# Optimization experiments

Measured on AMD Instinct MI355X. Metric: run time of the kernel, lower is better.

The kernel has to match this reference:

```python
import jax, jax.numpy as jnp
import numpy as np

DIM = 768; NL = 13; NH = 12; VOCAB = 50257; SEQ = 512; B = 4
HID = 4 * DIM; HD = DIM // NH; LUT_SIZE = 256


def setup_inputs() -> dict:
    key = jax.random.key(0)
    ks = jax.random.split(key, 10)
    def n(k, shape, s=0.02):
        return jax.random.normal(k, shape, jnp.float32) * s
    return {
        'lut': jnp.linspace(-0.1, 0.1, LUT_SIZE, dtype=jnp.float32),  # 256-entry primal codebook
        'tok_emb': n(ks[0], (VOCAB, DIM)),
        'pos_emb': n(ks[1], (SEQ, DIM)),
        'ln1_g': jnp.ones((NL, DIM), jnp.float32), 'ln1_b': jnp.zeros((NL, DIM), jnp.float32),
        'in_w': n(ks[2], (NL, 3 * DIM, DIM)), 'in_b': jnp.zeros((NL, 3 * DIM), jnp.float32),
        'out_w': n(ks[3], (NL, DIM, DIM)), 'out_b': jnp.zeros((NL, DIM), jnp.float32),
        'ln2_g': jnp.ones((NL, DIM), jnp.float32), 'ln2_b': jnp.zeros((NL, DIM), jnp.float32),
        'mlp1_scale': jnp.ones((NL, HID, 1), jnp.float32),
        'mlp2_scale': jnp.ones((NL, DIM, 1), jnp.float32),
        'lnf_g': jnp.ones((DIM,), jnp.float32), 'lnf_b': jnp.zeros((DIM,), jnp.float32),
        'head_scale': jnp.ones((VOCAB, 1), jnp.float32),
        'mlp1_idx': jax.random.randint(ks[4], (NL, HID, DIM), 0, LUT_SIZE, jnp.int32),
        'mlp2_idx': jax.random.randint(ks[5], (NL, DIM, HID), 0, LUT_SIZE, jnp.int32),
        'head_idx': jax.random.randint(ks[6], (VOCAB, DIM), 0, LUT_SIZE, jnp.int32),
        'idx': jax.random.randint(ks[7], (B, SEQ), 0, VOCAB, jnp.int32),
    }


def layernorm(x, g, b, eps=1e-5):
    m = jnp.mean(x, -1, keepdims=True)
    v = jnp.var(x, -1, keepdims=True)
    return (x - m) * jax.lax.rsqrt(v + eps) * g + b


def ghost_linear(x, gidx, scale, lut):
    # dequantize: gather codebook values, row-scale, then matmul (no bias)
    w = lut[gidx] * scale  # [out, in]
    return x @ w.T


def mha(x, wi, bi, wo, bo, mask):
    Bn, T, D = x.shape
    qkv = x @ wi.T + bi
    q, k, v = jnp.split(qkv, 3, axis=-1)
    q = q.reshape(Bn, T, NH, HD); k = k.reshape(Bn, T, NH, HD); v = v.reshape(Bn, T, NH, HD)
    s = jnp.einsum('bqhd,bkhd->bhqk', q, k) / jnp.sqrt(jnp.float32(HD)) + mask
    a = jax.nn.softmax(s, axis=-1)
    o = jnp.einsum('bhqk,bkhd->bqhd', a, v).reshape(Bn, T, D)
    return o @ wo.T + bo


def reference(lut, tok_emb, pos_emb, ln1_g, ln1_b, in_w, in_b, out_w, out_b,
              ln2_g, ln2_b, mlp1_scale, mlp2_scale, lnf_g, lnf_b, head_scale,
              mlp1_idx, mlp2_idx, head_idx, idx):
    Bn, T = idx.shape
    x = tok_emb[idx] + pos_emb[:T]
    causal = jnp.triu(jnp.ones((T, T), bool), 1)
    mask = jnp.where(causal, -jnp.inf, 0.0).astype(jnp.float32)
    for l in range(NL):
        h = layernorm(x, ln1_g[l], ln1_b[l])
        x = x + mha(h, in_w[l], in_b[l], out_w[l], out_b[l], mask)
        h = layernorm(x, ln2_g[l], ln2_b[l])
        h = ghost_linear(h, mlp1_idx[l], mlp1_scale[l], lut)
        h = jax.nn.gelu(h, approximate=True)  # GELU tanh approximation
        x = x + ghost_linear(h, mlp2_idx[l], mlp2_scale[l], lut)
    x = layernorm(x, lnf_g, lnf_b)
    return ghost_linear(x, head_idx, head_scale, lut)
```

## Files before the change

### kernel.cpp

```cpp
#include <hip/hip_runtime.h>
#include <stdint.h>

#define DIM 768
#define NL 13
#define NH 12
#define VOCAB 50257
#define SEQ 512
#define BATCH 4
#define HID 3072
#define HD 64
#define NTOK (BATCH*SEQ)
#define BHB (BATCH*NH)

typedef unsigned short u16;
typedef __attribute__((ext_vector_type(8))) __bf16 bf16x8;
typedef __attribute__((ext_vector_type(4))) float f32x4;

__device__ __forceinline__ u16 f2bf(float f) {
    union { float f; uint32_t u; } v; v.f = f;
    uint32_t u = v.u;
    return (u16)((u + 0x7FFFu + ((u >> 16) & 1u)) >> 16);
}

__device__ __forceinline__ void gl2lds16(const void* g, void* l) {
    __builtin_amdgcn_global_load_lds((const __attribute__((address_space(1))) void*)g,
                                     (__attribute__((address_space(3))) void*)l,
                                     16, 0, 0);
}

__device__ __forceinline__ float gelu_tanh(float x) {
    float x3 = x * x * x;
    float t = tanhf(0.7978845608028654f * (x + 0.044715f * x3));
    return 0.5f * x * (1.0f + t);
}

template<int EPI>
__device__ __forceinline__ void epi_store(float v, int r, int c, int N, int z, long sC,
                                          const float* bias, const float* resid,
                                          void* out0, void* out1, void* out2)
{
    if constexpr (EPI == 0) {
        if (c < N) ((float*)out0)[(long)z * sC + (long)r * N + c] = v;
    } else if constexpr (EPI == 1) {
        v += bias[c];
        const int part = c / DIM;
        const int cc = c - part * DIM;
        const int hh = cc >> 6, d = cc & 63;
        const int b = r >> 9, t = r & 511;
        const int bh = b * NH + hh;
        if (part == 0)      ((u16*)out0)[((long)bh * SEQ + t) * HD + d] = f2bf(v);
        else if (part == 1) ((u16*)out1)[((long)bh * SEQ + t) * HD + d] = f2bf(v);
        else                ((u16*)out2)[((long)bh * HD + d) * SEQ + t] = f2bf(v);
    } else if constexpr (EPI == 3) {
        if (bias) v += bias[c];
        v += resid[(long)r * N + c];
        ((float*)out0)[(long)r * N + c] = v;
    } else {
        ((u16*)out0)[(long)r * N + c] = f2bf(gelu_tanh(v));
    }
}

template<int WN, int EPI>
__global__ __launch_bounds__(256)
void gemm_bt(const u16* __restrict__ A, const u16* __restrict__ B,
             const float* __restrict__ bias, const float* __restrict__ resid,
             void* __restrict__ out0, void* __restrict__ out1, void* __restrict__ out2,
             int M, int N, int K, long sA, long sB, long sC)
{
    constexpr int TN = WN * 32;
    __shared__ __align__(16) u16 As[2 * 128 * 32];
    __shared__ __align__(16) u16 Bs[2 * TN * 32];

    const int tid  = threadIdx.x;
    const int wave = tid >> 6;
    const int lane = tid & 63;
    const int quad = lane >> 4;
    const int l16  = lane & 15;
    const int wm   = wave >> 1;
    const int wn   = wave & 1;

    int bx = blockIdx.x, by = blockIdx.y;
    {
        const int gx = gridDim.x;
        const int nwg = gx * gridDim.y;
        const int orig = by * gx + bx;
        const int xcd = orig & 7;
        const int q = nwg >> 3, r = nwg & 7;
        const int wg = (xcd < r ? xcd * (q + 1) : r * (q + 1) + (xcd - r) * q) + (orig >> 3);
        bx = wg % gx; by = wg / gx;
    }

    const int m0 = bx * 128;
    const int n0 = by * TN;
    const int z  = blockIdx.z;

    const u16* Ab = A + (long)z * sA;
    const u16* Bb = B + (long)z * sB;

    const int srow = tid >> 2;
    const int scol = ((tid & 3) ^ ((srow >> 1) & 3)) * 8;

    u16* const asw0 = As + wave * 512;
    u16* const asw1 = As + 2048 + wave * 512;
    u16* const bsw0 = Bs + wave * 512;
    u16* const bsw1 = Bs + 2048 + wave * 512;

    const long aoff0 = (long)(m0 + srow) * K + scol;
    const long aoff1 = (long)(m0 + 64 + srow) * K + scol;
    int br0 = n0 + srow;      if (br0 > N - 1) br0 = N - 1;
    int br1 = n0 + 64 + srow; if (br1 > N - 1) br1 = N - 1;
    const long boff0 = (long)br0 * K + scol;
    const long boff1 = (long)br1 * K + scol;

    auto stage = [&](int b, int k0) {
        const int ao = b * 4096;
        const int bo = b * (TN * 32);
        gl2lds16(Ab + aoff0 + k0, asw0 + ao);
        gl2lds16(Ab + aoff1 + k0, asw1 + ao);
        gl2lds16(Bb + boff0 + k0, bsw0 + bo);
        if constexpr (WN == 4) gl2lds16(Bb + boff1 + k0, bsw1 + bo);
    };

    f32x4 acc[4][WN];
    #pragma unroll
    for (int i = 0; i < 4; i++)
        #pragma unroll
        for (int j = 0; j < WN; j++)
            acc[i][j] = (f32x4){0.f, 0.f, 0.f, 0.f};

    const int sq8 = (quad ^ ((l16 >> 1) & 3)) * 8;
    const int arow = (wm * 64 + l16) * 32 + sq8;
    const int brow = (wn * (WN * 16) + l16) * 32 + sq8;

    stage(0, 0);
    __syncthreads();

    int cur = 0;
    for (int k0 = 0; k0 < K; k0 += 32) {
        if (k0 + 32 < K) stage(cur ^ 1, k0 + 32);

        const u16* Ar = As + cur * 4096;
        const u16* Br = Bs + cur * (TN * 32);
        bf16x8 af[4], bfr[WN];
        #pragma unroll
        for (int i = 0; i < 4; i++)
            af[i] = *(const bf16x8*)&Ar[arow + i * 512];
        #pragma unroll
        for (int j = 0; j < WN; j++)
            bfr[j] = *(const bf16x8*)&Br[brow + j * 512];
        #pragma unroll
        for (int i = 0; i < 4; i++)
            #pragma unroll
            for (int j = 0; j < WN; j++)
                acc[i][j] = __builtin_amdgcn_mfma_f32_16x16x32_bf16(af[i], bfr[j], acc[i][j], 0, 0, 0);

        __syncthreads();
        cur ^= 1;
    }

    const int rbase = m0 + wm * 64;
    const int cbase = n0 + wn * (WN * 16);
    #pragma unroll
    for (int i = 0; i < 4; i++)
        #pragma unroll
        for (int j = 0; j < WN; j++)
            #pragma unroll
            for (int rg = 0; rg < 4; rg++)
                epi_store<EPI>(acc[i][j][rg], rbase + i * 16 + quad * 4 + rg,
                               cbase + j * 16 + l16, N, z, sC, bias, resid, out0, out1, out2);
}

template<int WN, int EPI>
__global__ __launch_bounds__(256)
void gemm_bt_s(const u16* __restrict__ A, const u16* __restrict__ B,
               const float* __restrict__ bias, const float* __restrict__ resid,
               void* __restrict__ out0, void* __restrict__ out1, void* __restrict__ out2,
               int M, int N, int K)
{
    constexpr int TN = WN * 32;
    __shared__ __align__(16) u16 As[2 * 64 * 32];
    __shared__ __align__(16) u16 Bs[2 * TN * 32];

    const int tid  = threadIdx.x;
    const int wave = tid >> 6;
    const int lane = tid & 63;
    const int quad = lane >> 4;
    const int l16  = lane & 15;
    const int wm   = wave >> 1;
    const int wn   = wave & 1;

    int bx = blockIdx.x, by = blockIdx.y;
    {
        const int gx = gridDim.x;
        const int nwg = gx * gridDim.y;
        const int orig = by * gx + bx;
        const int xcd = orig & 7;
        const int q = nwg >> 3, r = nwg & 7;
        const int wg = (xcd < r ? xcd * (q + 1) : r * (q + 1) + (xcd - r) * q) + (orig >> 3);
        bx = wg % gx; by = wg / gx;
    }

    const int m0 = bx * 64;
    const int n0 = by * TN;

    const int srow = tid >> 2;
    const int scol = ((tid & 3) ^ ((srow >> 1) & 3)) * 8;

    u16* const asw  = As + wave * 512;
    u16* const bsw0 = Bs + wave * 512;
    u16* const bsw1 = Bs + 2048 + wave * 512;

    const long aoff = (long)(m0 + srow) * K + scol;
    int br0 = n0 + srow;      if (br0 > N - 1) br0 = N - 1;
    int br1 = n0 + 64 + srow; if (br1 > N - 1) br1 = N - 1;
    const long boff0 = (long)br0 * K + scol;
    const long boff1 = (long)br1 * K + scol;

    auto stage = [&](int b, int k0) {
        gl2lds16(A + aoff + k0, asw + b * 2048);
        gl2lds16(B + boff0 + k0, bsw0 + b * (TN * 32));
        if constexpr (WN == 4) gl2lds16(B + boff1 + k0, bsw1 + b * (TN * 32));
    };

    f32x4 acc[2][WN];
    #pragma unroll
    for (int i = 0; i < 2; i++)
        #pragma unroll
        for (int j = 0; j < WN; j++)
            acc[i][j] = (f32x4){0.f, 0.f, 0.f, 0.f};

    const int sq8 = (quad ^ ((l16 >> 1) & 3)) * 8;
    const int arow = (wm * 32 + l16) * 32 + sq8;
    const int brow = (wn * (WN * 16) + l16) * 32 + sq8;

    stage(0, 0);
    __syncthreads();

    int cur = 0;
    for (int k0 = 0; k0 < K; k0 += 32) {
        if (k0 + 32 < K) stage(cur ^ 1, k0 + 32);

        const u16* Ar = As + cur * 2048;
        const u16* Br = Bs + cur * (TN * 32);
        bf16x8 af[2], bfr[WN];
        #pragma unroll
        for (int i = 0; i < 2; i++)
            af[i] = *(const bf16x8*)&Ar[arow + i * 512];
        #pragma unroll
        for (int j = 0; j < WN; j++)
            bfr[j] = *(const bf16x8*)&Br[brow + j * 512];
        #pragma unroll
        for (int i = 0; i < 2; i++)
            #pragma unroll
            for (int j = 0; j < WN; j++)
                acc[i][j] = __builtin_amdgcn_mfma_f32_16x16x32_bf16(af[i], bfr[j], acc[i][j], 0, 0, 0);

        __syncthreads();
        cur ^= 1;
    }

    const int rbase = m0 + wm * 32;
    const int cbase = n0 + wn * (WN * 16);
    #pragma unroll
    for (int i = 0; i < 2; i++)
        #pragma unroll
        for (int j = 0; j < WN; j++)
            #pragma unroll
            for (int rg = 0; rg < 4; rg++)
                epi_store<EPI>(acc[i][j][rg], rbase + i * 16 + quad * 4 + rg,
                               cbase + j * 16 + l16, N, 0, 0, bias, resid, out0, out1, out2);
}

__global__ __launch_bounds__(256)
void attn_kernel(const u16* __restrict__ qb, const u16* __restrict__ kb,
                 const u16* __restrict__ vtb, u16* __restrict__ ob)
{
    __shared__ __align__(16) u16 Ks[512 * 64];
    __shared__ __align__(16) u16 Vs[64 * 512];
    __shared__ __align__(16) u16 Ps[4][32 * 64];

    const int tid  = threadIdx.x;
    const int wave = tid >> 6;
    const int lane = tid & 63;
    const int quad = lane >> 4;
    const int l16  = lane & 15;

    const int bh   = blockIdx.x;
    const int qblk = blockIdx.y;
    const int qr0  = qblk * 128 + wave * 32;

    #pragma unroll 4
    for (int cI = 0; cI < 16; ++cI) {
        const int rbase = cI * 32 + wave * 8;
        const int r  = rbase + (lane >> 3);
        const int ch = lane & 7;
        gl2lds16(kb + ((long)bh * SEQ + r) * HD + ((ch ^ (r & 7)) * 8), Ks + rbase * 64);
    }
    #pragma unroll 4
    for (int cI = 0; cI < 16; ++cI) {
        const int d = cI * 4 + wave;
        gl2lds16(vtb + ((long)bh * HD + d) * SEQ + ((lane ^ (d & 7)) * 8), Vs + d * 512);
    }

    bf16x8 af[2][2];
    const long qoff = ((long)bh * SEQ + qr0) * HD;
    #pragma unroll
    for (int i = 0; i < 2; i++)
        #pragma unroll
        for (int kc = 0; kc < 2; kc++)
            af[i][kc] = *(const bf16x8*)&qb[qoff + (long)(i * 16 + l16) * HD + kc * 32 + quad * 8];

    __syncthreads();

    f32x4 o[2][4];
    float mrun[2][4], lrun[2][4];
    #pragma unroll
    for (int i = 0; i < 2; i++)
        #pragma unroll
        for (int rg = 0; rg < 4; rg++) { mrun[i][rg] = -1e30f; lrun[i][rg] = 0.f; }
    #pragma unroll
    for (int i = 0; i < 2; i++)
        #pragma unroll
        for (int nd = 0; nd < 4; nd++)
            o[i][nd] = (f32x4){0.f, 0.f, 0.f, 0.f};

    u16* const Pw = &Ps[wave][0];
    const int rsw = l16 & 7;
    const int kvend = qr0 + 32;

    for (int kv0 = 0; kv0 < kvend; kv0 += 64) {
        f32x4 s[2][4];
        #pragma unroll
        for (int i = 0; i < 2; i++)
            #pragma unroll
            for (int n = 0; n < 4; n++)
                s[i][n] = (f32x4){0.f, 0.f, 0.f, 0.f};
        bf16x8 bf[4][2];
        #pragma unroll
        for (int n = 0; n < 4; n++)
            #pragma unroll
            for (int kc = 0; kc < 2; kc++)
                bf[n][kc] = *(const bf16x8*)&Ks[(kv0 + n * 16 + l16) * 64 + (((kc * 4 + quad) ^ rsw) * 8)];
        #pragma unroll
        for (int i = 0; i < 2; i++)
            #pragma unroll
            for (int n = 0; n < 4; n++)
                #pragma unroll
                for (int kc = 0; kc < 2; kc++)
                    s[i][n] = __builtin_amdgcn_mfma_f32_16x16x32_bf16(af[i][kc], bf[n][kc], s[i][n], 0, 0, 0);

        #pragma unroll
        for (int i = 0; i < 2; i++) {
            #pragma unroll
            for (int rg = 0; rg < 4; rg++) {
                const int q = qr0 + i * 16 + quad * 4 + rg;
                float v[4];
                #pragma unroll
                for (int n = 0; n < 4; n++) {
                    const int c = kv0 + n * 16 + l16;
                    v[n] = (c <= q) ? s[i][n][rg] * 0.125f : -1e30f;
                }
                float pm = fmaxf(fmaxf(v[0], v[1]), fmaxf(v[2], v[3]));
                #pragma unroll
                for (int off = 1; off < 16; off <<= 1) pm = fmaxf(pm, __shfl_xor(pm, off));
                const float mo = mrun[i][rg];
                const float mn = fmaxf(mo, pm);
                const float corr = __expf(mo - mn);
                float ps = 0.f;
                #pragma unroll
                for (int n = 0; n < 4; n++) { const float e = __expf(v[n] - mn); v[n] = e; ps += e; }
                #pragma unroll
                for (int off = 1; off < 16; off <<= 1) ps += __shfl_xor(ps, off);
                lrun[i][rg] = lrun[i][rg] * corr + ps;
                mrun[i][rg] = mn;
                #pragma unroll
                for (int nd = 0; nd < 4; nd++) o[i][nd][rg] *= corr;
                const int qlz = i * 16 + quad * 4 + rg;
                const int sw = qlz & 7;
                #pragma unroll
                for (int n = 0; n < 4; n++)
                    Pw[qlz * 64 + (((n * 2 + (l16 >> 3)) ^ sw) * 8) + (l16 & 7)] = f2bf(v[n]);
            }
        }
        asm volatile("s_waitcnt lgkmcnt(0)" ::: "memory");

        bf16x8 pa[2][2], vb[4][2];
        #pragma unroll
        for (int i = 0; i < 2; i++)
            #pragma unroll
            for (int kc = 0; kc < 2; kc++)
                pa[i][kc] = *(const bf16x8*)&Pw[(i * 16 + l16) * 64 + (((kc * 4 + quad) ^ rsw) * 8)];
        #pragma unroll
        for (int nd = 0; nd < 4; nd++)
            #pragma unroll
            for (int kc = 0; kc < 2; kc++)
                vb[nd][kc] = *(const bf16x8*)&Vs[(nd * 16 + l16) * 512 + ((((kv0 >> 3) + kc * 4 + quad) ^ rsw) * 8)];
        #pragma unroll
        for (int i = 0; i < 2; i++)
            #pragma unroll
            for (int nd = 0; nd < 4; nd++)
                #pragma unroll
                for (int kc = 0; kc < 2; kc++)
                    o[i][nd] = __builtin_amdgcn_mfma_f32_16x16x32_bf16(pa[i][kc], vb[nd][kc], o[i][nd], 0, 0, 0);
    }

    const int b  = bh / NH, hh = bh - b * NH;
    #pragma unroll
    for (int i = 0; i < 2; i++) {
        #pragma unroll
        for (int rg = 0; rg < 4; rg++) {
            const float inv = 1.f / lrun[i][rg];
            const int t = qr0 + i * 16 + quad * 4 + rg;
            u16* orow = ob + ((long)(b * SEQ + t)) * DIM + hh * HD;
            #pragma unroll
            for (int nd = 0; nd < 4; nd++)
                orow[nd * 16 + l16] = f2bf(o[i][nd][rg] * inv);
        }
    }
}

__global__ __launch_bounds__(256)
void embed_kernel(const int* __restrict__ tokidx, const float* __restrict__ tok,
                  const float* __restrict__ pos, float* __restrict__ x)
{
    const int i = blockIdx.x * 256 + threadIdx.x;
    const int row = i / 192;
    const int c4 = i - row * 192;
    const int t = row & (SEQ - 1);
    const int tk = tokidx[row];
    const float4 a = *(const float4*)&tok[(long)tk * DIM + c4 * 4];
    const float4 p = *(const float4*)&pos[(long)t * DIM + c4 * 4];
    *(float4*)&x[(long)row * DIM + c4 * 4] = make_float4(a.x + p.x, a.y + p.y, a.z + p.z, a.w + p.w);
}

__global__ __launch_bounds__(256)
void ln_kernel(const float* __restrict__ x, const float* __restrict__ g,
               const float* __restrict__ b, u16* __restrict__ out)
{
    const int row = blockIdx.x * 4 + (threadIdx.x >> 6);
    const int lane = threadIdx.x & 63;
    const float* xr = x + (long)row * DIM;
    float v[12];
    float s = 0.f, s2 = 0.f;
    #pragma unroll
    for (int i = 0; i < 3; i++) {
        const float4 f = *(const float4*)&xr[i * 256 + lane * 4];
        v[i*4+0] = f.x; v[i*4+1] = f.y; v[i*4+2] = f.z; v[i*4+3] = f.w;
        s  += f.x + f.y + f.z + f.w;
        s2 += f.x*f.x + f.y*f.y + f.z*f.z + f.w*f.w;
    }
    for (int o = 32; o; o >>= 1) { s += __shfl_xor(s, o); s2 += __shfl_xor(s2, o); }
    const float m  = s * (1.f / DIM);
    const float var = s2 * (1.f / DIM) - m * m;
    const float rs = rsqrtf(var + 1e-5f);
    u16* orow = out + (long)row * DIM;
    #pragma unroll
    for (int i = 0; i < 3; i++) {
        const int c = i * 256 + lane * 4;
        ushort4 o4 = make_ushort4(
            f2bf((v[i*4+0] - m) * rs * g[c+0] + b[c+0]),
            f2bf((v[i*4+1] - m) * rs * g[c+1] + b[c+1]),
            f2bf((v[i*4+2] - m) * rs * g[c+2] + b[c+2]),
            f2bf((v[i*4+3] - m) * rs * g[c+3] + b[c+3]));
        *(ushort4*)&orow[c] = o4;
    }
}

__global__ __launch_bounds__(256)
void tobf16_kernel(const float* __restrict__ in, u16* __restrict__ out)
{
    const long i = ((long)blockIdx.x * 256 + threadIdx.x) * 4;
    const float4 f = *(const float4*)&in[i];
    *(ushort4*)&out[i] = make_ushort4(f2bf(f.x), f2bf(f.y), f2bf(f.z), f2bf(f.w));
}

__global__ __launch_bounds__(256)
void dequant_kernel(const int* __restrict__ gidx, const float* __restrict__ scale,
                    const float* __restrict__ lut, u16* __restrict__ w,
                    long total, int Kd)
{
    __shared__ float slut[256];
    slut[threadIdx.x] = lut[threadIdx.x];
    __syncthreads();
    const long i4 = ((long)blockIdx.x * 256 + threadIdx.x) * 4;
    if (i4 >= total) return;
    const int4 g = *(const int4*)&gidx[i4];
    const float sc = scale[(int)(i4 / Kd)];
    *(ushort4*)&w[i4] = make_ushort4(f2bf(slut[g.x] * sc), f2bf(slut[g.y] * sc),
                                     f2bf(slut[g.z] * sc), f2bf(slut[g.w] * sc));
}

extern "C" void kernel_launch(void* const* d_in, const int* in_sizes, int n_in,
                              void* d_out, int out_size, void* d_ws, size_t ws_size,
                              hipStream_t stream)
{
    const float* lut        = (const float*)d_in[0];
    const float* tok_emb    = (const float*)d_in[1];
    const float* pos_emb    = (const float*)d_in[2];
    const float* ln1_g      = (const float*)d_in[3];
    const float* ln1_b      = (const float*)d_in[4];
    const float* in_w       = (const float*)d_in[5];
    const float* in_b       = (const float*)d_in[6];
    const float* out_w      = (const float*)d_in[7];
    const float* out_b      = (const float*)d_in[8];
    const float* ln2_g      = (const float*)d_in[9];
    const float* ln2_b      = (const float*)d_in[10];
    const float* mlp1_scale = (const float*)d_in[11];
    const float* mlp2_scale = (const float*)d_in[12];
    const float* lnf_g      = (const float*)d_in[13];
    const float* lnf_b      = (const float*)d_in[14];
    const float* head_scale = (const float*)d_in[15];
    const int*   mlp1_idx   = (const int*)d_in[16];
    const int*   mlp2_idx   = (const int*)d_in[17];
    const int*   head_idx   = (const int*)d_in[18];
    const int*   tokids     = (const int*)d_in[19];

    char* p = (char*)d_ws;
    auto alloc = [&](size_t bytes) { char* r = p; p += (bytes + 255) & ~(size_t)255; return r; };
    float* x    = (float*)alloc((size_t)NTOK * DIM * 4);
    u16*  h     = (u16*) alloc((size_t)NTOK * DIM * 2);
    u16*  h2    = (u16*) alloc((size_t)NTOK * HID * 2);
    u16*  qb    = (u16*) alloc((size_t)BHB * SEQ * HD * 2);
    u16*  kb    = (u16*) alloc((size_t)BHB * SEQ * HD * 2);
    u16*  vtb   = (u16*) alloc((size_t)BHB * SEQ * HD * 2);
    u16*  ob    = (u16*) alloc((size_t)NTOK * DIM * 2);
    u16*  inw16 = (u16*) alloc((size_t)NL * 3 * DIM * DIM * 2);
    u16*  outw16= (u16*) alloc((size_t)NL * DIM * DIM * 2);
    u16*  w1    = (u16*) alloc((size_t)HID * DIM * 2);
    u16*  w2    = (u16*) alloc((size_t)DIM * HID * 2);
    u16*  hw    = (u16*) alloc((size_t)VOCAB * DIM * 2);

    embed_kernel<<<NTOK * 192 / 256, 256, 0, stream>>>(tokids, tok_emb, pos_emb, x);
    tobf16_kernel<<<NL * 3 * DIM * DIM / 1024, 256, 0, stream>>>(in_w, inw16);
    tobf16_kernel<<<NL * DIM * DIM / 1024, 256, 0, stream>>>(out_w, outw16);
    {
        const long total = (long)VOCAB * DIM;
        const int blocks = (int)((total / 4 + 255) / 256);
        dequant_kernel<<<blocks, 256, 0, stream>>>(head_idx, head_scale, lut, hw, total, DIM);
    }

    for (int l = 0; l < NL; l++) {
        ln_kernel<<<NTOK / 4, 256, 0, stream>>>(x, ln1_g + l * DIM, ln1_b + l * DIM, h);
        gemm_bt_s<4, 1><<<dim3(NTOK / 64, 3 * DIM / 128), 256, 0, stream>>>(
            h, inw16 + (long)l * 3 * DIM * DIM, in_b + l * 3 * DIM, nullptr,
            qb, kb, vtb, NTOK, 3 * DIM, DIM);
        attn_kernel<<<dim3(BHB, 4), 256, 0, stream>>>(qb, kb, vtb, ob);
        gemm_bt_s<2, 3><<<dim3(NTOK / 64, DIM / 64), 256, 0, stream>>>(
            ob, outw16 + (long)l * DIM * DIM, out_b + l * DIM, x,
            x, nullptr, nullptr, NTOK, DIM, DIM);
        ln_kernel<<<NTOK / 4, 256, 0, stream>>>(x, ln2_g + l * DIM, ln2_b + l * DIM, h);
        dequant_kernel<<<HID * DIM / 1024, 256, 0, stream>>>(
            mlp1_idx + (long)l * HID * DIM, mlp1_scale + l * HID, lut, w1, (long)HID * DIM, DIM);
        gemm_bt_s<4, 4><<<dim3(NTOK / 64, HID / 128), 256, 0, stream>>>(
            h, w1, nullptr, nullptr, h2, nullptr, nullptr, NTOK, HID, DIM);
        dequant_kernel<<<DIM * HID / 1024, 256, 0, stream>>>(
            mlp2_idx + (long)l * DIM * HID, mlp2_scale + l * DIM, lut, w2, (long)DIM * HID, HID);
        gemm_bt_s<2, 3><<<dim3(NTOK / 64, DIM / 64), 256, 0, stream>>>(
            h2, w2, nullptr, x, x, nullptr, nullptr, NTOK, DIM, HID);
    }

    ln_kernel<<<NTOK / 4, 256, 0, stream>>>(x, lnf_g, lnf_b, h);
    gemm_bt<4, 0><<<dim3(NTOK / 128, (VOCAB + 127) / 128, 1), 256, 0, stream>>>(
        h, hw, nullptr, nullptr, d_out, nullptr, nullptr, NTOK, VOCAB, DIM, 0, 0, 0);
}
```

Measured before the change: 2.935 ms.

## Fuse LUT dequantization into MLP GEMMs and widen K-tile to 64

Removes the separate per-layer dequant kernels for the MLP weights. The GEMM now loads int32 codebook indices straight from global memory, looks them up in an LDS-resident LUT, applies the row scale, converts to bf16 and writes the result into shared memory, with the loads software-pipelined against the MFMA loop. The K tile grows from 32 to 64 with a new 8-way XOR swizzle, which halves the number of barriers per K. In exchange, every M-tile block re-reads and re-dequantizes the int32 indices, which are 4 bytes per weight, so global traffic for the weights rises unless L2 absorbs it.

Result: slower. 3.222 ms (+9.8%).

```diff
diff --git a/kernel.cpp b/kernel.cpp
--- a/kernel.cpp
+++ b/kernel.cpp
@@ -32,6 +32,16 @@
     float x3 = x * x * x;
     float t = tanhf(0.7978845608028654f * (x + 0.044715f * x3));
     return 0.5f * x * (1.0f + t);
+}
+
+__device__ __forceinline__ void xcd_remap(int& bx, int& by) {
+    const int gx = gridDim.x;
+    const int nwg = gx * gridDim.y;
+    const int orig = by * gx + bx;
+    const int xcd = orig & 7;
+    const int q = nwg >> 3, r = nwg & 7;
+    const int wg = (xcd < r ? xcd * (q + 1) : r * (q + 1) + (xcd - r) * q) + (orig >> 3);
+    bx = wg % gx; by = wg / gx;
 }
 
 template<int EPI>
@@ -80,15 +90,7 @@
     const int wn   = wave & 1;
 
     int bx = blockIdx.x, by = blockIdx.y;
-    {
-        const int gx = gridDim.x;
-        const int nwg = gx * gridDim.y;
-        const int orig = by * gx + bx;
-        const int xcd = orig & 7;
-        const int q = nwg >> 3, r = nwg & 7;
-        const int wg = (xcd < r ? xcd * (q + 1) : r * (q + 1) + (xcd - r) * q) + (orig >> 3);
-        bx = wg % gx; by = wg / gx;
-    }
+    xcd_remap(bx, by);
 
     const int m0 = bx * 128;
     const int n0 = by * TN;
@@ -170,16 +172,19 @@
                                cbase + j * 16 + l16, N, z, sC, bias, resid, out0, out1, out2);
 }
 
-template<int WN, int EPI>
+template<int WN, int EPI, bool GHOST>
 __global__ __launch_bounds__(256)
-void gemm_bt_s(const u16* __restrict__ A, const u16* __restrict__ B,
-               const float* __restrict__ bias, const float* __restrict__ resid,
-               void* __restrict__ out0, void* __restrict__ out1, void* __restrict__ out2,
-               int M, int N, int K)
+void gemm64(const u16* __restrict__ A, const void* __restrict__ Bsrc,
+            const float* __restrict__ scale, const float* __restrict__ lutg,
+            const float* __restrict__ bias, const float* __restrict__ resid,
+            void* __restrict__ out0, void* __restrict__ out1, void* __restrict__ out2,
+            int M, int N, int K)
 {
     constexpr int TN = WN * 32;
-    __shared__ __align__(16) u16 As[2 * 64 * 32];
-    __shared__ __align__(16) u16 Bs[2 * TN * 32];
+    constexpr int NC = TN / 32;
+    __shared__ __align__(16) u16 As[2 * 64 * 64];
+    __shared__ __align__(16) u16 Bs[2 * TN * 64];
+    __shared__ float slut[256];
 
     const int tid  = threadIdx.x;
     const int wave = tid >> 6;
@@ -190,36 +195,59 @@
     const int wn   = wave & 1;
 
     int bx = blockIdx.x, by = blockIdx.y;
-    {
-        const int gx = gridDim.x;
-        const int nwg = gx * gridDim.y;
-        const int orig = by * gx + bx;
-        const int xcd = orig & 7;
-        const int q = nwg >> 3, r = nwg & 7;
-        const int wg = (xcd < r ? xcd * (q + 1) : r * (q + 1) + (xcd - r) * q) + (orig >> 3);
-        bx = wg % gx; by = wg / gx;
-    }
-
+    xcd_remap(bx, by);
     const int m0 = bx * 64;
     const int n0 = by * TN;
 
-    const int srow = tid >> 2;
-    const int scol = ((tid & 3) ^ ((srow >> 1) & 3)) * 8;
-
-    u16* const asw  = As + wave * 512;
-    u16* const bsw0 = Bs + wave * 512;
-    u16* const bsw1 = Bs + 2048 + wave * 512;
-
-    const long aoff = (long)(m0 + srow) * K + scol;
-    int br0 = n0 + srow;      if (br0 > N - 1) br0 = N - 1;
-    int br1 = n0 + 64 + srow; if (br1 > N - 1) br1 = N - 1;
-    const long boff0 = (long)br0 * K + scol;
-    const long boff1 = (long)br1 * K + scol;
-
-    auto stage = [&](int b, int k0) {
-        gl2lds16(A + aoff + k0, asw + b * 2048);
-        gl2lds16(B + boff0 + k0, bsw0 + b * (TN * 32));
-        if constexpr (WN == 4) gl2lds16(B + boff1 + k0, bsw1 + b * (TN * 32));
+    if constexpr (GHOST) slut[tid] = lutg[tid];
+
+    const int srow = tid >> 3;
+    const int sch  = ((tid & 7) ^ (srow & 7)) * 8;
+    u16* const asw = As + wave * 512;
+
+    const long aoff = (long)(m0 + srow) * K + sch;
+    auto stageA = [&](int b, int k0) {
+        #pragma unroll
+        for (int c = 0; c < 2; c++)
+            gl2lds16(A + aoff + (long)c * 32 * K + k0, asw + b * 4096 + c * 2048);
+    };
+
+    const u16* const Bw = (const u16*)Bsrc;
+    u16* const bsw = Bs + wave * 512;
+    const long boff = (long)(n0 + srow) * K + sch;
+    auto stageB = [&](int b, int k0) {
+        #pragma unroll
+        for (int c = 0; c < NC; c++)
+            gl2lds16(Bw + boff + (long)c * 32 * K + k0, bsw + b * TN * 64 + c * 2048);
+    };
+
+    const int* const gidx = (const int*)Bsrc;
+    int4 gq[NC][2];
+    float bsc[NC];
+    if constexpr (GHOST) {
+        #pragma unroll
+        for (int c = 0; c < NC; c++) bsc[c] = scale[n0 + c * 32 + srow];
+    }
+    auto ghostLoad = [&](int k0) {
+        #pragma unroll
+        for (int c = 0; c < NC; c++) {
+            const long o = (long)(n0 + c * 32 + srow) * K + k0 + (tid & 7) * 8;
+            gq[c][0] = *(const int4*)&gidx[o];
+            gq[c][1] = *(const int4*)&gidx[o + 4];
+        }
+    };
+    auto ghostWrite = [&](int b) {
+        #pragma unroll
+        for (int c = 0; c < NC; c++) {
+            const float s = bsc[c];
+            uint32_t p0 = (uint32_t)f2bf(slut[gq[c][0].x] * s) | ((uint32_t)f2bf(slut[gq[c][0].y] * s) << 16);
+            uint32_t p1 = (uint32_t)f2bf(slut[gq[c][0].z] * s) | ((uint32_t)f2bf(slut[gq[c][0].w] * s) << 16);
+            uint32_t p2 = (uint32_t)f2bf(slut[gq[c][1].x] * s) | ((uint32_t)f2bf(slut[gq[c][1].y] * s) << 16);
+            uint32_t p3 = (uint32_t)f2bf(slut[gq[c][1].z] * s) | ((uint32_t)f2bf(slut[gq[c][1].w] * s) << 16);
+            u16* dst = Bs + b * TN * 64 + (c * 32 + srow) * 64 + sch;
+            uint4 w; w.x = p0; w.y = p1; w.z = p2; w.w = p3;
+            *(uint4*)dst = w;
+        }
     };
 
     f32x4 acc[2][WN];
@@ -229,32 +257,50 @@
         for (int j = 0; j < WN; j++)
             acc[i][j] = (f32x4){0.f, 0.f, 0.f, 0.f};
 
-    const int sq8 = (quad ^ ((l16 >> 1) & 3)) * 8;
-    const int arow = (wm * 32 + l16) * 32 + sq8;
-    const int brow = (wn * (WN * 16) + l16) * 32 + sq8;
-
-    stage(0, 0);
-    __syncthreads();
+    const int rsw = l16 & 7;
+
+    stageA(0, 0);
+    if constexpr (GHOST) {
+        ghostLoad(0);
+        __syncthreads();
+        ghostWrite(0);
+        __syncthreads();
+    } else {
+        stageB(0, 0);
+        __syncthreads();
+    }
 
     int cur = 0;
-    for (int k0 = 0; k0 < K; k0 += 32) {
-        if (k0 + 32 < K) stage(cur ^ 1, k0 + 32);
-
-        const u16* Ar = As + cur * 2048;
-        const u16* Br = Bs + cur * (TN * 32);
-        bf16x8 af[2], bfr[WN];
+    for (int k0 = 0; k0 < K; k0 += 64) {
+        const bool more = (k0 + 64 < K);
+        if (more) {
+            stageA(cur ^ 1, k0 + 64);
+            if constexpr (GHOST) ghostLoad(k0 + 64);
+            else stageB(cur ^ 1, k0 + 64);
+        }
+
+        const u16* Ar = As + cur * 4096;
+        const u16* Br = Bs + cur * TN * 64;
+        bf16x8 af[2][2], bfr[WN][2];
         #pragma unroll
         for (int i = 0; i < 2; i++)
-            af[i] = *(const bf16x8*)&Ar[arow + i * 512];
+            #pragma unroll
+            for (int kk = 0; kk < 2; kk++)
+                af[i][kk] = *(const bf16x8*)&Ar[(wm * 32 + i * 16 + l16) * 64 + (((kk * 4 + quad) ^ rsw) * 8)];
         #pragma unroll
         for (int j = 0; j < WN; j++)
-            bfr[j] = *(const bf16x8*)&Br[brow + j * 512];
-        #pragma unroll
-        for (int i = 0; i < 2; i++)
-            #pragma unroll
-            for (int j = 0; j < WN; j++)
-                acc[i][j] = __builtin_amdgcn_mfma_f32_16x16x32_bf16(af[i], bfr[j], acc[i][j], 0, 0, 0);
-
+            #pragma unroll
+            for (int kk = 0; kk < 2; kk++)
+                bfr[j][kk] = *(const bf16x8*)&Br[(wn * (WN * 16) + j * 16 + l16) * 64 + (((kk * 4 + quad) ^ rsw) * 8)];
+        #pragma unroll
+        for (int kk = 0; kk < 2; kk++)
+            #pragma unroll
+            for (int i = 0; i < 2; i++)
+                #pragma unroll
+                for (int j = 0; j < WN; j++)
+                    acc[i][j] = __builtin_amdgcn_mfma_f32_16x16x32_bf16(af[i][kk], bfr[j][kk], acc[i][j], 0, 0, 0);
+
+        if constexpr (GHOST) { if (more) ghostWrite(cur ^ 1); }
         __syncthreads();
         cur ^= 1;
     }
@@ -526,8 +572,6 @@
     u16*  ob    = (u16*) alloc((size_t)NTOK * DIM * 2);
     u16*  inw16 = (u16*) alloc((size_t)NL * 3 * DIM * DIM * 2);
     u16*  outw16= (u16*) alloc((size_t)NL * DIM * DIM * 2);
-    u16*  w1    = (u16*) alloc((size_t)HID * DIM * 2);
-    u16*  w2    = (u16*) alloc((size_t)DIM * HID * 2);
     u16*  hw    = (u16*) alloc((size_t)VOCAB * DIM * 2);
 
     embed_kernel<<<NTOK * 192 / 256, 256, 0, stream>>>(tokids, tok_emb, pos_emb, x);
@@ -541,22 +585,20 @@
 
     for (int l = 0; l < NL; l++) {
         ln_kernel<<<NTOK / 4, 256, 0, stream>>>(x, ln1_g + l * DIM, ln1_b + l * DIM, h);
-        gemm_bt_s<4, 1><<<dim3(NTOK / 64, 3 * DIM / 128), 256, 0, stream>>>(
-            h, inw16 + (long)l * 3 * DIM * DIM, in_b + l * 3 * DIM, nullptr,
+        gemm64<4, 1, false><<<dim3(NTOK / 64, 3 * DIM / 128), 256, 0, stream>>>(
+            h, inw16 + (long)l * 3 * DIM * DIM, nullptr, lut, in_b + l * 3 * DIM, nullptr,
             qb, kb, vtb, NTOK, 3 * DIM, DIM);
         attn_kernel<<<dim3(BHB, 4), 256, 0, stream>>>(qb, kb, vtb, ob);
-        gemm_bt_s<2, 3><<<dim3(NTOK / 64, DIM / 64), 256, 0, stream>>>(
-            ob, outw16 + (long)l * DIM * DIM, out_b + l * DIM, x,
+        gemm64<2, 3, false><<<dim3(NTOK / 64, DIM / 64), 256, 0, stream>>>(
+            ob, outw16 + (long)l * DIM * DIM, nullptr, lut, out_b + l * DIM, x,
             x, nullptr, nullptr, NTOK, DIM, DIM);
         ln_kernel<<<NTOK / 4, 256, 0, stream>>>(x, ln2_g + l * DIM, ln2_b + l * DIM, h);
-        dequant_kernel<<<HID * DIM / 1024, 256, 0, stream>>>(
-            mlp1_idx + (long)l * HID * DIM, mlp1_scale + l * HID, lut, w1, (long)HID * DIM, DIM);
-        gemm_bt_s<4, 4><<<dim3(NTOK / 64, HID / 128), 256, 0, stream>>>(
-            h, w1, nullptr, nullptr, h2, nullptr, nullptr, NTOK, HID, DIM);
-        dequant_kernel<<<DIM * HID / 1024, 256, 0, stream>>>(
-            mlp2_idx + (long)l * DIM * HID, mlp2_scale + l * DIM, lut, w2, (long)DIM * HID, HID);
-        gemm_bt_s<2, 3><<<dim3(NTOK / 64, DIM / 64), 256, 0, stream>>>(
-            h2, w2, nullptr, x, x, nullptr, nullptr, NTOK, DIM, HID);
+        gemm64<4, 4, true><<<dim3(NTOK / 64, HID / 128), 256, 0, stream>>>(
+            h, mlp1_idx + (long)l * HID * DIM, mlp1_scale + l * HID, lut, nullptr, nullptr,
+            h2, nullptr, nullptr, NTOK, HID, DIM);
+        gemm64<2, 3, true><<<dim3(NTOK / 64, DIM / 64), 256, 0, stream>>>(
+            h2, mlp2_idx + (long)l * DIM * HID, mlp2_scale + l * DIM, lut, nullptr, x,
+            x, nullptr, nullptr, NTOK, DIM, HID);
     }
 
     ln_kernel<<<NTOK / 4, 256, 0, stream>>>(x, lnf_g, lnf_b, h);
```
